# Performance work log

Hardware: AMD Instinct MI355X
Metric: run time of the kernel (lower is better)

Reference implementation:

```python
import jax, jax.numpy as jnp
import numpy as np

B, H, S, DK = 2, 16, 2048, 64


def setup_inputs() -> dict:
    key = jax.random.key(0)
    kq, kk, kv = jax.random.split(key, 3)
    q = jax.random.normal(kq, (B, H, S, DK), dtype=jnp.float32)
    k = jax.random.normal(kk, (B, H, S, DK), dtype=jnp.float32)
    v = jax.random.normal(kv, (B, H, S, DK), dtype=jnp.float32)
    # 3-D boolean mask [B, Sq, Sk]; True = allowed. Causal lower-triangular.
    mask = jnp.broadcast_to(jnp.tril(jnp.ones((S, S), dtype=bool)), (B, S, S))
    return {"q": q, "k": k, "v": v, "mask": mask}


def reference(q, k, v, mask):
    # scores: [B, H, Sq, Sk]
    scores = jnp.einsum("bhqd,bhkd->bhqk", q, k) / jnp.sqrt(jnp.asarray(DK, q.dtype))
    if mask.ndim == scores.ndim - 1:
        mask = mask[:, None, :, :]  # broadcast over heads
    scores = jnp.where(mask, scores, jnp.asarray(-jnp.inf, scores.dtype))
    attn = jax.nn.softmax(scores, axis=-1)
    out = jnp.einsum("bhqk,bhkd->bhqd", attn, v)
    return out
```

## Files before the change

kernel.cpp:

```cpp
#include <hip/hip_runtime.h>


typedef float    v4f __attribute__((ext_vector_type(4)));
typedef _Float16 v4h __attribute__((ext_vector_type(4)));
typedef _Float16 v8h __attribute__((ext_vector_type(8)));

#define SEQ 2048
#define DKC 64

#if __has_builtin(__builtin_amdgcn_exp2f)
#define EXP2(x) __builtin_amdgcn_exp2f(x)
#else
#define EXP2(x) exp2f(x)
#endif

#define MFMA16(a,b,c) __builtin_amdgcn_mfma_f32_16x16x16f16(a,b,c,0,0,0)
#define MFMA32(a,b,c) __builtin_amdgcn_mfma_f32_16x16x32_f16(a,b,c,0,0,0)

__global__ __launch_bounds__(256) void prep_kv(const float* __restrict__ k,
                                               const float* __restrict__ v,
                                               _Float16* __restrict__ kh,
                                               _Float16* __restrict__ vt) {
  const int bh = blockIdx.x;
  const int kt = blockIdx.y;
  const int tid = threadIdx.x;
  {
    const int quad = tid & 3;
    const int l16  = (tid >> 2) & 15;
    const int st   = (tid >> 6) & 1;
    const int s    = tid >> 7;
    const float* src = k + ((size_t)bh * SEQ + kt * 32 + s * 16 + l16) * DKC + st * 32 + quad * 8;
    float4 a = *(const float4*)src;
    float4 b = *(const float4*)(src + 4);
    v8h h;
    h[0] = (_Float16)a.x; h[1] = (_Float16)a.y; h[2] = (_Float16)a.z; h[3] = (_Float16)a.w;
    h[4] = (_Float16)b.x; h[5] = (_Float16)b.y; h[6] = (_Float16)b.z; h[7] = (_Float16)b.w;
    *(v8h*)(kh + (size_t)bh * SEQ * DKC
               + (size_t)(kt * 4 + s * 2 + st) * 512 + l16 * 32 + quad * 8) = h;
  }
  {
    const int d = tid & 63, q4 = tid >> 6;
    const float* src = v + ((size_t)bh * SEQ + kt * 32) * DKC + d;
    v8h h;
#pragma unroll
    for (int j = 0; j < 4; ++j) h[j]     = (_Float16)src[(size_t)(q4 * 4 + j) * DKC];
#pragma unroll
    for (int j = 0; j < 4; ++j) h[4 + j] = (_Float16)src[(size_t)(16 + q4 * 4 + j) * DKC];
    *(v8h*)(vt + (size_t)bh * SEQ * DKC + (size_t)kt * 2048
               + (d >> 4) * 512 + (q4 * 16 + (d & 15)) * 8) = h;
  }
}

__device__ __forceinline__ void load_chunk(const _Float16* __restrict__ khl,
                                           const _Float16* __restrict__ vtl,
                                           int kt, v8h (&kf)[4], v8h (&va)[4]) {
  const _Float16* kp = khl + (size_t)kt * 2048;
  const _Float16* vp = vtl + (size_t)kt * 2048;
#pragma unroll
  for (int i = 0; i < 4; ++i) kf[i] = *(const v8h*)(kp + i * 512);
#pragma unroll
  for (int i = 0; i < 4; ++i) va[i] = *(const v8h*)(vp + i * 512);
}

__device__ __forceinline__ void compute_chunk(int kt, int wkt, int qw, int l16, int quad,
                                              const v8h (&qf)[2][2],
                                              const v8h (&kf)[4], const v8h (&va)[4],
                                              v4f (&O)[2][4], v4f (&L)[2], const v4h ones) {
  v4f S[2][2] = {};
#pragma unroll
  for (int t = 0; t < 2; ++t)
#pragma unroll
    for (int s = 0; s < 2; ++s) {
      S[t][s] = MFMA32(kf[s * 2 + 0], qf[t][0], S[t][s]);
      S[t][s] = MFMA32(kf[s * 2 + 1], qf[t][1], S[t][s]);
    }

  if (kt == wkt - 1) {
    const int k0 = kt * 32;
#pragma unroll
    for (int t = 0; t < 2; ++t) {
      const int qg = qw + t * 16 + l16;
#pragma unroll
      for (int s = 0; s < 2; ++s) {
        const int kb = k0 + s * 16 + quad * 4;
#pragma unroll
        for (int r = 0; r < 4; ++r)
          if (kb + r > qg) S[t][s][r] = -3e38f;
      }
    }
  }

  v4h pf[2][2];
#pragma unroll
  for (int t = 0; t < 2; ++t)
#pragma unroll
    for (int s = 0; s < 2; ++s) {
      v4h p;
#pragma unroll
      for (int r = 0; r < 4; ++r) p[r] = (_Float16)EXP2(S[t][s][r]);
      pf[t][s] = p;
    }

#pragma unroll
  for (int dc = 0; dc < 4; ++dc) {
    v4h lo = __builtin_shufflevector(va[dc], va[dc], 0, 1, 2, 3);
    v4h hi = __builtin_shufflevector(va[dc], va[dc], 4, 5, 6, 7);
    O[0][dc] = MFMA16(lo, pf[0][0], O[0][dc]);
    O[0][dc] = MFMA16(hi, pf[0][1], O[0][dc]);
    O[1][dc] = MFMA16(lo, pf[1][0], O[1][dc]);
    O[1][dc] = MFMA16(hi, pf[1][1], O[1][dc]);
  }
  L[0] = MFMA16(ones, pf[0][0], L[0]);
  L[0] = MFMA16(ones, pf[0][1], L[0]);
  L[1] = MFMA16(ones, pf[1][0], L[1]);
  L[1] = MFMA16(ones, pf[1][1], L[1]);
}

__global__ __launch_bounds__(128, 2) void fa_fwd(const float* __restrict__ q,
                                                 const _Float16* __restrict__ kh,
                                                 const _Float16* __restrict__ vt,
                                                 float* __restrict__ out) {
  __shared__ v4f lbuf[10][64];

  const int lane = threadIdx.x & 63;
  const int wid  = threadIdx.x >> 6;
  const int quad = lane >> 4;
  const int l16  = lane & 15;

  const int g  = (int)blockIdx.x & 7;
  const int r  = (int)blockIdx.x >> 3;
  const int bh = g * 4 + (r & 3);
  const int pr = r >> 2;

  const size_t base = (size_t)bh * SEQ * DKC;
  const _Float16* khl = kh + base + l16 * 32 + quad * 8;
  const _Float16* vtl = vt + base + (quad * 16 + l16) * 8;

  const float CSC = 0.18033688011112042f;
  const v4h ones = {(_Float16)1.f, (_Float16)1.f, (_Float16)1.f, (_Float16)1.f};

#pragma unroll
  for (int ph = 0; ph < 2; ++ph) {
    const int qp  = ph ? (63 - pr) : pr;
    const int qw  = qp * 32;
    const int wkt = qp + 1;
    const int h   = (wkt + 1) >> 1;
    const int kb  = wid ? h : 0;
    const int ke  = wid ? wkt : h;

    v8h qf[2][2];
#pragma unroll
    for (int t = 0; t < 2; ++t)
#pragma unroll
      for (int st = 0; st < 2; ++st) {
        const float* qr = q + base + (size_t)(qw + t * 16 + l16) * DKC + st * 32 + quad * 8;
        float4 a = *(const float4*)qr;
        float4 b = *(const float4*)(qr + 4);
        v8h hq;
        hq[0] = (_Float16)(a.x * CSC); hq[1] = (_Float16)(a.y * CSC);
        hq[2] = (_Float16)(a.z * CSC); hq[3] = (_Float16)(a.w * CSC);
        hq[4] = (_Float16)(b.x * CSC); hq[5] = (_Float16)(b.y * CSC);
        hq[6] = (_Float16)(b.z * CSC); hq[7] = (_Float16)(b.w * CSC);
        qf[t][st] = hq;
      }

    v4f O[2][4] = {};
    v4f L[2]    = {};

    if (kb < ke) {
      v8h kfA[4], kfB[4], vaA[4], vaB[4];
      load_chunk(khl, vtl, kb, kfA, vaA);
      int kt = kb;
      while (true) {
        if (kt + 1 < ke) load_chunk(khl, vtl, kt + 1, kfB, vaB);
        compute_chunk(kt, wkt, qw, l16, quad, qf, kfA, vaA, O, L, ones);
        if (++kt >= ke) break;
        if (kt + 1 < ke) load_chunk(khl, vtl, kt + 1, kfA, vaA);
        compute_chunk(kt, wkt, qw, l16, quad, qf, kfB, vaB, O, L, ones);
        if (++kt >= ke) break;
      }
    }

    __syncthreads();
    if (wid == 0) {
#pragma unroll
      for (int t = 0; t < 2; ++t) {
#pragma unroll
        for (int dc = 0; dc < 4; ++dc) lbuf[t * 4 + dc][lane] = O[t][dc];
        lbuf[8 + t][lane] = L[t];
      }
    }
    __syncthreads();
    if (wid == 1) {
#pragma unroll
      for (int t = 0; t < 2; ++t) {
#pragma unroll
        for (int dc = 0; dc < 4; ++dc) O[t][dc] += lbuf[t * 4 + dc][lane];
        L[t] += lbuf[8 + t][lane];
      }
#pragma unroll
      for (int t = 0; t < 2; ++t) {
        const float inv = 1.0f / L[t][0];
        float* orow = out + base + (size_t)(qw + t * 16 + l16) * DKC + quad * 4;
#pragma unroll
        for (int dc = 0; dc < 4; ++dc) {
          float4 w;
          w.x = O[t][dc][0] * inv; w.y = O[t][dc][1] * inv;
          w.z = O[t][dc][2] * inv; w.w = O[t][dc][3] * inv;
          *(float4*)(orow + dc * 16) = w;
        }
      }
    }
  }
}

extern "C" void kernel_launch(void* const* d_in, const int* in_sizes, int n_in,
                              void* d_out, int out_size, void* d_ws, size_t ws_size,
                              hipStream_t stream) {
  (void)in_sizes; (void)n_in; (void)out_size; (void)ws_size;
  const float* q = (const float*)d_in[0];
  const float* k = (const float*)d_in[1];
  const float* v = (const float*)d_in[2];
  float* out = (float*)d_out;

  _Float16* kh = (_Float16*)d_ws;
  _Float16* vt = (_Float16*)((char*)d_ws + (size_t)32 * SEQ * DKC * 2);

  prep_kv<<<dim3(32, 64), dim3(256), 0, stream>>>(k, v, kh, vt);
  fa_fwd<<<dim3(1024), dim3(128), 0, stream>>>(q, kh, vt, out);
}
```

Measured before the change: 135.0 us.

## Share K/V tiles across four waves via async global-to-LDS double buffering

Replaces per-wave direct global loads of K/V with block-cooperative global_load_lds staging into double-buffered shared memory. Each 256-thread block now covers 128 query rows, with each wave owning 32, so one K/V tile is reused by four waves. This drops the old two-wave split of the key range and the LDS reduction of partial results. The K layout is changed so LDS reads are lane-contiguous. The grid shrinks to 256 blocks, which lowers parallelism and adds per-chunk barriers, and waves with shorter causal ranges sit idle while others finish.

```diff
diff --git a/kernel.cpp b/kernel.cpp
--- a/kernel.cpp
+++ b/kernel.cpp
@@ -36,7 +36,7 @@
     h[0] = (_Float16)a.x; h[1] = (_Float16)a.y; h[2] = (_Float16)a.z; h[3] = (_Float16)a.w;
     h[4] = (_Float16)b.x; h[5] = (_Float16)b.y; h[6] = (_Float16)b.z; h[7] = (_Float16)b.w;
     *(v8h*)(kh + (size_t)bh * SEQ * DKC
-               + (size_t)(kt * 4 + s * 2 + st) * 512 + l16 * 32 + quad * 8) = h;
+               + (size_t)(kt * 4 + s * 2 + st) * 512 + (quad * 16 + l16) * 8) = h;
   }
   {
     const int d = tid & 63, q4 = tid >> 6;
@@ -51,18 +51,7 @@
   }
 }
 
-__device__ __forceinline__ void load_chunk(const _Float16* __restrict__ khl,
-                                           const _Float16* __restrict__ vtl,
-                                           int kt, v8h (&kf)[4], v8h (&va)[4]) {
-  const _Float16* kp = khl + (size_t)kt * 2048;
-  const _Float16* vp = vtl + (size_t)kt * 2048;
-#pragma unroll
-  for (int i = 0; i < 4; ++i) kf[i] = *(const v8h*)(kp + i * 512);
-#pragma unroll
-  for (int i = 0; i < 4; ++i) va[i] = *(const v8h*)(vp + i * 512);
-}
-
-__device__ __forceinline__ void compute_chunk(int kt, int wkt, int qw, int l16, int quad,
+__device__ __forceinline__ void compute_chunk(int k0, bool straddle, int qw, int l16, int quad,
                                               const v8h (&qf)[2][2],
                                               const v8h (&kf)[4], const v8h (&va)[4],
                                               v4f (&O)[2][4], v4f (&L)[2], const v4h ones) {
@@ -75,8 +64,7 @@
       S[t][s] = MFMA32(kf[s * 2 + 1], qf[t][1], S[t][s]);
     }
 
-  if (kt == wkt - 1) {
-    const int k0 = kt * 32;
+  if (straddle) {
 #pragma unroll
     for (int t = 0; t < 2; ++t) {
       const int qg = qw + t * 16 + l16;
@@ -116,14 +104,29 @@
   L[1] = MFMA16(ones, pf[1][1], L[1]);
 }
 
-__global__ __launch_bounds__(128, 2) void fa_fwd(const float* __restrict__ q,
-                                                 const _Float16* __restrict__ kh,
-                                                 const _Float16* __restrict__ vt,
-                                                 float* __restrict__ out) {
-  __shared__ v4f lbuf[10][64];
+#define GLD16(gp, lp) __builtin_amdgcn_global_load_lds(                     \
+    (const __attribute__((address_space(1))) void*)(gp),                    \
+    (__attribute__((address_space(3))) void*)(lp), 16, 0, 0)
+
+#define STAGE(bf, c) do {                                                   \
+    const char* _gk = khb + (size_t)(c) * 16384 + w * 4096 + lane * 16;     \
+    const char* _gv = vtb + (size_t)(c) * 16384 + w * 4096 + lane * 16;     \
+    char* _lk = ((char*)&lds[bf][0][0]) + w * 4096;                         \
+    char* _lv = ((char*)&lds[bf][1][0]) + w * 4096;                         \
+    GLD16(_gk,        _lk);        GLD16(_gk + 1024, _lk + 1024);           \
+    GLD16(_gk + 2048, _lk + 2048); GLD16(_gk + 3072, _lk + 3072);           \
+    GLD16(_gv,        _lv);        GLD16(_gv + 1024, _lv + 1024);           \
+    GLD16(_gv + 2048, _lv + 2048); GLD16(_gv + 3072, _lv + 3072);           \
+  } while (0)
+
+__global__ __launch_bounds__(256) void fa_fwd(const float* __restrict__ q,
+                                              const _Float16* __restrict__ kh,
+                                              const _Float16* __restrict__ vt,
+                                              float* __restrict__ out) {
+  __shared__ _Float16 lds[2][2][8192];
 
   const int lane = threadIdx.x & 63;
-  const int wid  = threadIdx.x >> 6;
+  const int w    = threadIdx.x >> 6;
   const int quad = lane >> 4;
   const int l16  = lane & 15;
 
@@ -133,20 +136,18 @@
   const int pr = r >> 2;
 
   const size_t base = (size_t)bh * SEQ * DKC;
-  const _Float16* khl = kh + base + l16 * 32 + quad * 8;
-  const _Float16* vtl = vt + base + (quad * 16 + l16) * 8;
+  const char* khb = (const char*)(kh + base);
+  const char* vtb = (const char*)(vt + base);
 
   const float CSC = 0.18033688011112042f;
   const v4h ones = {(_Float16)1.f, (_Float16)1.f, (_Float16)1.f, (_Float16)1.f};
 
 #pragma unroll
   for (int ph = 0; ph < 2; ++ph) {
-    const int qp  = ph ? (63 - pr) : pr;
-    const int qw  = qp * 32;
-    const int wkt = qp + 1;
-    const int h   = (wkt + 1) >> 1;
-    const int kb  = wid ? h : 0;
-    const int ke  = wid ? wkt : h;
+    const int qb  = ph ? (15 - pr) : pr;
+    const int qw  = qb * 128 + w * 32;
+    const int myk = qw >> 5;
+    const int NC  = qb + 1;
 
     v8h qf[2][2];
 #pragma unroll
@@ -167,48 +168,37 @@
     v4f O[2][4] = {};
     v4f L[2]    = {};
 
-    if (kb < ke) {
-      v8h kfA[4], kfB[4], vaA[4], vaB[4];
-      load_chunk(khl, vtl, kb, kfA, vaA);
-      int kt = kb;
-      while (true) {
-        if (kt + 1 < ke) load_chunk(khl, vtl, kt + 1, kfB, vaB);
-        compute_chunk(kt, wkt, qw, l16, quad, qf, kfA, vaA, O, L, ones);
-        if (++kt >= ke) break;
-        if (kt + 1 < ke) load_chunk(khl, vtl, kt + 1, kfA, vaA);
-        compute_chunk(kt, wkt, qw, l16, quad, qf, kfB, vaB, O, L, ones);
-        if (++kt >= ke) break;
-      }
-    }
-
+    STAGE(0, 0);
     __syncthreads();
-    if (wid == 0) {
-#pragma unroll
-      for (int t = 0; t < 2; ++t) {
-#pragma unroll
-        for (int dc = 0; dc < 4; ++dc) lbuf[t * 4 + dc][lane] = O[t][dc];
-        lbuf[8 + t][lane] = L[t];
-      }
-    }
-    __syncthreads();
-    if (wid == 1) {
-#pragma unroll
-      for (int t = 0; t < 2; ++t) {
-#pragma unroll
-        for (int dc = 0; dc < 4; ++dc) O[t][dc] += lbuf[t * 4 + dc][lane];
-        L[t] += lbuf[8 + t][lane];
-      }
-#pragma unroll
-      for (int t = 0; t < 2; ++t) {
-        const float inv = 1.0f / L[t][0];
-        float* orow = out + base + (size_t)(qw + t * 16 + l16) * DKC + quad * 4;
-#pragma unroll
-        for (int dc = 0; dc < 4; ++dc) {
-          float4 w;
-          w.x = O[t][dc][0] * inv; w.y = O[t][dc][1] * inv;
-          w.z = O[t][dc][2] * inv; w.w = O[t][dc][3] * inv;
-          *(float4*)(orow + dc * 16) = w;
+
+    for (int c = 0; c < NC; ++c) {
+      if (c + 1 < NC) STAGE((c + 1) & 1, c + 1);
+      const int b = c & 1;
+#pragma unroll
+      for (int kl = 0; kl < 4; ++kl) {
+        const int kt32 = c * 4 + kl;
+        if (kt32 <= myk) {
+          v8h kf[4], va[4];
+#pragma unroll
+          for (int i = 0; i < 4; ++i) kf[i] = *(const v8h*)&lds[b][0][kl * 2048 + i * 512 + lane * 8];
+#pragma unroll
+          for (int i = 0; i < 4; ++i) va[i] = *(const v8h*)&lds[b][1][kl * 2048 + i * 512 + lane * 8];
+          compute_chunk(kt32 * 32, kt32 == myk, qw, l16, quad, qf, kf, va, O, L, ones);
         }
+      }
+      __syncthreads();
+    }
+
+#pragma unroll
+    for (int t = 0; t < 2; ++t) {
+      const float inv = 1.0f / L[t][0];
+      float* orow = out + base + (size_t)(qw + t * 16 + l16) * DKC + quad * 4;
+#pragma unroll
+      for (int dc = 0; dc < 4; ++dc) {
+        float4 o;
+        o.x = O[t][dc][0] * inv; o.y = O[t][dc][1] * inv;
+        o.z = O[t][dc][2] * inv; o.w = O[t][dc][3] * inv;
+        *(float4*)(orow + dc * 16) = o;
       }
     }
   }
@@ -227,5 +217,5 @@
   _Float16* vt = (_Float16*)((char*)d_ws + (size_t)32 * SEQ * DKC * 2);
 
   prep_kv<<<dim3(32, 64), dim3(256), 0, stream>>>(k, v, kh, vt);
-  fa_fwd<<<dim3(1024), dim3(128), 0, stream>>>(q, kh, vt, out);
-}
+  fa_fwd<<<dim3(256), dim3(256), 0, stream>>>(q, kh, vt, out);
+}
```

New measurement: 144.7 us. 7.2% more time.
